# Performance work log

Measured on AMD Instinct MI355X. Metric: run time of the kernel, lower is better.

The kernel has to match this reference:

```python
import jax, jax.numpy as jnp
import numpy as np

B = 16384   # number of cells
SD = 1024   # spatial_dim
TD = 1024   # temporal_dim
FD = 1024   # fusion_dim
H = 8       # num_attention_heads


def setup_inputs() -> dict:
    key = jax.random.key(0)
    ks = jax.random.split(key, 40)
    it = iter(range(40))

    def w(o, i):
        return jax.random.normal(ks[next(it)], (o, i), dtype=jnp.float32) * 0.02

    def b(o):
        return jnp.zeros((o,), dtype=jnp.float32)

    d = {
        "spatial_features": jax.random.normal(ks[next(it)], (B, SD), dtype=jnp.float32),
        "temporal_features": jax.random.normal(ks[next(it)], (B, TD), dtype=jnp.float32),
        "sp_w": w(FD, SD), "sp_b": b(FD),
        "tp_w": w(FD, TD), "tp_b": b(FD),
    }
    for pre in ("st", "ts", "sa"):  # spatial->temporal, temporal->spatial, self
        for nm in ("q", "k", "v", "o"):
            d[f"{pre}_{nm}w"] = w(FD, FD)
            d[f"{pre}_{nm}b"] = b(FD)
    d["f1_w"] = w(FD, 2 * FD); d["f1_b"] = b(FD)
    d["f2_w"] = w(FD, FD);     d["f2_b"] = b(FD)
    d["ln_g"] = jnp.ones((FD,), jnp.float32)
    d["ln_b"] = jnp.zeros((FD,), jnp.float32)
    return d


def _mha(xq, xk, xv, qw, qb, kw, kb, vw, vb, ow, ob):
    # xq: [B, Lq, D]; xk/xv: [B, Lk, D]
    Bx, Lq, D = xq.shape
    Lk = xk.shape[1]
    hd = D // H
    Q = (xq @ qw.T + qb).reshape(Bx, Lq, H, hd)
    K = (xk @ kw.T + kb).reshape(Bx, Lk, H, hd)
    V = (xv @ vw.T + vb).reshape(Bx, Lk, H, hd)
    scores = jnp.einsum("bqhd,bkhd->bhqk", Q, K) / jnp.sqrt(jnp.float32(hd))
    attn = jax.nn.softmax(scores, axis=-1)
    out = jnp.einsum("bhqk,bkhd->bqhd", attn, V).reshape(Bx, Lq, D)
    return out @ ow.T + ob


def reference(spatial_features, temporal_features,
              sp_w, sp_b, tp_w, tp_b,
              st_qw, st_qb, st_kw, st_kb, st_vw, st_vb, st_ow, st_ob,
              ts_qw, ts_qb, ts_kw, ts_kb, ts_vw, ts_vb, ts_ow, ts_ob,
              sa_qw, sa_qb, sa_kw, sa_kb, sa_vw, sa_vb, sa_ow, sa_ob,
              f1_w, f1_b, f2_w, f2_b, ln_g, ln_b):
    # projections to fusion dim, add seq_len=1 axis
    sp = (spatial_features @ sp_w.T + sp_b)[:, None, :]   # [B,1,F]
    tp = (temporal_features @ tp_w.T + tp_b)[:, None, :]  # [B,1,F]

    # cross attention
    s_att = _mha(sp, tp, tp, st_qw, st_qb, st_kw, st_kb, st_vw, st_vb, st_ow, st_ob)[:, 0, :]
    t_att = _mha(tp, sp, sp, ts_qw, ts_qb, ts_kw, ts_kb, ts_vw, ts_vb, ts_ow, ts_ob)[:, 0, :]

    # concat fusion MLP
    cat = jnp.concatenate([s_att, t_att], axis=-1)        # [B,2F]
    fused = jax.nn.relu(cat @ f1_w.T + f1_b) @ f2_w.T + f2_b

    # self attention over seq_len=1
    fe = fused[:, None, :]
    fused = _mha(fe, fe, fe, sa_qw, sa_qb, sa_kw, sa_kb, sa_vw, sa_vb, sa_ow, sa_ob)[:, 0, :]

    # layer norm (eps matches torch default 1e-5)
    mu = jnp.mean(fused, axis=-1, keepdims=True)
    var = jnp.mean(jnp.square(fused - mu), axis=-1, keepdims=True)
    return (fused - mu) * jax.lax.rsqrt(var + 1e-5) * ln_g + ln_b
```

## Files before the change

### kernel.cpp

```cpp
#include <hip/hip_runtime.h>
#include <hip/hip_fp16.h>


typedef _Float16 half8 __attribute__((ext_vector_type(8)));
typedef float floatx4 __attribute__((ext_vector_type(4)));

#define GLOBAL_AS __attribute__((address_space(1)))
#define LDS_AS __attribute__((address_space(3)))

#define NB 16384
#define FDIM 1024

#define SBAR() asm volatile("s_barrier" ::: "memory")
#define WAIT_LGKM0() asm volatile("s_waitcnt lgkmcnt(0)" ::: "memory")
#define WAIT_VM(n) asm volatile("s_waitcnt vmcnt(" #n ")" ::: "memory")
#define SB0() __builtin_amdgcn_sched_barrier(0)
#define DSREAD(dst, addr) asm volatile("ds_read_b128 %0, %1" : "=v"(dst) : "v"(addr))

template <int RELU>
__global__ __launch_bounds__(512, 2) void gemm256(
    const _Float16* __restrict__ A, const _Float16* __restrict__ W,
    const float* __restrict__ bias, _Float16* __restrict__ C,
    int M, int N, int K, int ldc) {
  __shared__ __align__(16) _Float16 smem[2 * 2 * 256 * 64];

  const int t = threadIdx.x;
  const int lane = t & 63;
  const int w = t >> 6;
  const int wr = w >> 2;
  const int wc = w & 3;

  const int nwg = gridDim.x;
  const int bid = blockIdx.x;
  const int swz = (bid & 7) * (nwg >> 3) + (bid >> 3);
  const int nTN = N >> 8;
  const int m0 = (swz / nTN) << 8;
  const int n0 = (swz % nTN) << 8;
  const int NT = K >> 6;

  const int srow = w * 16 + (lane >> 3);
  const int scs = (lane & 7) ^ ((lane >> 3) & 7);
  const char* gA = (const char*)(A + (long)(m0 + srow) * K + scs * 8);
  const char* gB = (const char*)(W + (long)(n0 + srow) * K + scs * 8);
  const long dJ = (long)K * 16;
  const long dH = (long)K * 256;
  const int ldst = w * 2048 + lane * 16;

  unsigned sb = (unsigned)(unsigned long long)(LDS_AS void*)smem;
  const int frow = lane & 15;
  const unsigned offk = (unsigned)((((lane >> 4) * 16) ^ ((frow & 7) << 4)));
  const unsigned aoff = (unsigned)((wr * 128 + frow) * 128);
  const unsigned boff = (unsigned)(32768 + (wc * 64 + frow) * 128);

  floatx4 acc[8][4] = {};
  half8 b[4][2], aP[2][2], aQ[2][2];

#define STAGE(ab, hf, buf, gp, kb)                                               \
  do {                                                                           \
    const char* _s = (gp) + (hf) * dH + (kb);                                    \
    char* _d = (char*)smem + (buf) * 65536 + (ab) * 32768 + (hf) * 16384 + ldst; \
    __builtin_amdgcn_global_load_lds((const GLOBAL_AS void*)_s,                  \
                                     (LDS_AS void*)_d, 16, 0, 0);                \
    __builtin_amdgcn_global_load_lds((const GLOBAL_AS void*)(_s + dJ),           \
                                     (LDS_AS void*)(_d + 1024), 16, 0, 0);       \
  } while (0)

#define RD_B()                                                                    \
  do {                                                                            \
    _Pragma("unroll") for (int c = 0; c < 4; ++c) {                               \
      DSREAD(b[c][0], baseB + c * 2048 + offk);                                   \
      DSREAD(b[c][1], baseB + c * 2048 + (offk ^ 64u));                           \
    }                                                                             \
  } while (0)

#define RD_A(S, r, ba)                                                            \
  do {                                                                            \
    DSREAD(S[0][0], (ba) + (r) * 2048 + offk);                                    \
    DSREAD(S[0][1], (ba) + (r) * 2048 + (offk ^ 64u));                            \
    DSREAD(S[1][0], (ba) + (r + 1) * 2048 + offk);                                \
    DSREAD(S[1][1], (ba) + (r + 1) * 2048 + (offk ^ 64u));                        \
  } while (0)

#define QUAD(S, i0, i1)                                                                     \
  do {                                                                                      \
    __builtin_amdgcn_s_setprio(1);                                                          \
    _Pragma("unroll") for (int c = 0; c < 4; ++c) {                                         \
      acc[i0][c] = __builtin_amdgcn_mfma_f32_16x16x32_f16(S[0][0], b[c][0], acc[i0][c], 0, 0, 0); \
      acc[i0][c] = __builtin_amdgcn_mfma_f32_16x16x32_f16(S[0][1], b[c][1], acc[i0][c], 0, 0, 0); \
      acc[i1][c] = __builtin_amdgcn_mfma_f32_16x16x32_f16(S[1][0], b[c][0], acc[i1][c], 0, 0, 0); \
      acc[i1][c] = __builtin_amdgcn_mfma_f32_16x16x32_f16(S[1][1], b[c][1], acc[i1][c], 0, 0, 0); \
    }                                                                                       \
    __builtin_amdgcn_s_setprio(0);                                                          \
  } while (0)

  {
    const long k1 = 128L;
    STAGE(0, 0, 0, gA, 0); STAGE(0, 1, 0, gA, 0);
    STAGE(1, 0, 0, gB, 0); STAGE(1, 1, 0, gB, 0);
    STAGE(1, 0, 1, gB, k1); STAGE(1, 1, 1, gB, k1);
  }
  WAIT_VM(4);
  SBAR();
  RD_A(aP, 0, sb + aoff);

  for (int kt = 0; kt < NT; ++kt) {
    const int cur = kt & 1, nxt = cur ^ 1;
    const unsigned baseA = sb + (unsigned)(cur * 65536) + aoff;
    const unsigned baseAn = sb + (unsigned)(nxt * 65536) + aoff;
    const unsigned baseB = sb + (unsigned)(cur * 65536) + boff;
    const long kb1 = (long)(kt + 1 < NT ? kt + 1 : NT - 1) * 128;
    const long kb2 = (long)(kt + 2 < NT ? kt + 2 : NT - 1) * 128;

    RD_B();
    STAGE(0, 0, nxt, gA, kb1);
    SBAR(); WAIT_LGKM0();
    RD_A(aQ, 2, baseA);
    SB0();
    QUAD(aP, 0, 1);
    SBAR();

    STAGE(0, 1, nxt, gA, kb1);
    SBAR(); WAIT_LGKM0();
    RD_A(aP, 4, baseA);
    SB0();
    QUAD(aQ, 2, 3);
    SBAR();

    STAGE(1, 0, cur, gB, kb2);
    SBAR(); WAIT_LGKM0();
    RD_A(aQ, 6, baseA);
    SB0();
    QUAD(aP, 4, 5);
    SBAR();

    STAGE(1, 1, cur, gB, kb2);
    WAIT_VM(4);
    SBAR(); WAIT_LGKM0();
    RD_A(aP, 0, baseAn);
    SB0();
    QUAD(aQ, 6, 7);
    SBAR();
  }
  WAIT_VM(0);
  WAIT_LGKM0();

  const int rbase = (lane >> 4) * 4;
#pragma unroll
  for (int c = 0; c < 4; ++c) {
    const int col = n0 + wc * 64 + c * 16 + frow;
    const float bv = bias[col];
#pragma unroll
    for (int r = 0; r < 8; ++r) {
#pragma unroll
      for (int j = 0; j < 4; ++j) {
        int row = m0 + wr * 128 + r * 16 + rbase + j;
        float v = acc[r][c][j] + bv;
        if (RELU) v = fmaxf(v, 0.f);
        C[(long)row * ldc + col] = (_Float16)v;
      }
    }
  }
#undef STAGE
#undef RD_B
#undef RD_A
#undef QUAD
}

struct CVE { const float* in; _Float16* out; long ld_in; long ld_out; long n4; };
struct CVB { CVE e[7]; };
__global__ __launch_bounds__(256) void cvt_batch(CVB a) {
  const CVE e = a.e[blockIdx.y];
  long i = (long)blockIdx.x * blockDim.x + threadIdx.x;
  long stride = (long)gridDim.x * blockDim.x;
  for (; i < e.n4; i += stride) {
    long row = i >> 8;
    long c4 = i & 255;
    float4 v = *reinterpret_cast<const float4*>(e.in + row * e.ld_in + c4 * 4);
    union { _Float16 h[4]; short4 s; } u;
    u.h[0] = (_Float16)v.x; u.h[1] = (_Float16)v.y;
    u.h[2] = (_Float16)v.z; u.h[3] = (_Float16)v.w;
    *reinterpret_cast<short4*>(e.out + row * e.ld_out + c4 * 4) = u.s;
  }
}

struct TP8 { const float* in[8]; _Float16* out[8]; };
__global__ __launch_bounds__(256) void transpose_cvt(TP8 args) {
  __shared__ float tile[32][33];
  const float* in = args.in[blockIdx.z];
  _Float16* out = args.out[blockIdx.z];
  const int bx = blockIdx.x * 32;
  const int by = blockIdx.y * 32;
  const int tx = threadIdx.x & 31;
  const int ty = threadIdx.x >> 5;
#pragma unroll
  for (int r = 0; r < 32; r += 8)
    tile[ty + r][tx] = in[(long)(by + ty + r) * 1024 + bx + tx];
  __syncthreads();
#pragma unroll
  for (int r = 0; r < 32; r += 8)
    out[(long)(bx + ty + r) * 1024 + by + tx] = (_Float16)tile[tx][ty + r];
}

struct MVE { const float* W; const float* x; const float* add; float* y; long ld; int kj; };
struct MVB { MVE e[3]; };
__global__ __launch_bounds__(256) void matvecb(MVB a) {
  const MVE e = a.e[blockIdx.y];
  const int row = blockIdx.x * 4 + (threadIdx.x >> 6);
  const int lane = threadIdx.x & 63;
  const float* wr = e.W + (long)row * e.ld;
  float s = 0.f;
  for (int j = 0; j < e.kj; ++j) {
    float4 w4 = *reinterpret_cast<const float4*>(wr + (lane + 64 * j) * 4);
    float4 x4 = *reinterpret_cast<const float4*>(e.x + (lane + 64 * j) * 4);
    s += w4.x * x4.x + w4.y * x4.y + w4.z * x4.z + w4.w * x4.w;
  }
#pragma unroll
  for (int off = 32; off > 0; off >>= 1) s += __shfl_down(s, off);
  if (lane == 0) e.y[row] = s + (e.add ? e.add[row] : 0.f);
}

struct GemmArgs { const _Float16* A; const _Float16* W; const float* bias; _Float16* C; int ldc; };
struct GB5 { GemmArgs g[5]; };

__global__ __launch_bounds__(256, 2) void gemm_f16(GB5 args, int M, int N, int K) {
  __shared__ __align__(16) _Float16 As[128 * 32];
  __shared__ __align__(16) _Float16 Ws[128 * 32];

  const GemmArgs ga = args.g[blockIdx.y];
  const int t = threadIdx.x;
  const int lane = t & 63;
  const int wave = t >> 6;
  const int wr = wave >> 1;
  const int wc = wave & 1;

  const int nwg = gridDim.x;
  const int bid = blockIdx.x;
  const int swz = (bid & 7) * (nwg >> 3) + (bid >> 3);
  const int nTilesN = N >> 7;
  const int m0 = (swz / nTilesN) << 7;
  const int n0 = (swz % nTilesN) << 7;

  floatx4 acc[4][4] = {};
  const int srow = t >> 2;
  const int scol = (t & 3) * 8;
  const _Float16* Ag = ga.A + (long)(m0 + srow) * K + scol;
  const _Float16* Wg = ga.W + (long)(n0 + srow) * K + scol;
  const int frow = lane & 15;
  const int fk = (lane >> 4) * 8;

  for (int k0 = 0; k0 < K; k0 += 32) {
#pragma unroll
    for (int i = 0; i < 2; ++i) {
      __builtin_amdgcn_global_load_lds(
          (const GLOBAL_AS void*)(Ag + (long)i * 64 * K + k0),
          (LDS_AS void*)(&As[i * 2048 + t * 8]), 16, 0, 0);
      __builtin_amdgcn_global_load_lds(
          (const GLOBAL_AS void*)(Wg + (long)i * 64 * K + k0),
          (LDS_AS void*)(&Ws[i * 2048 + t * 8]), 16, 0, 0);
    }
    __syncthreads();
    half8 a[4], b[4];
#pragma unroll
    for (int r = 0; r < 4; ++r)
      a[r] = *(const half8*)&As[(wr * 64 + r * 16 + frow) * 32 + fk];
#pragma unroll
    for (int c = 0; c < 4; ++c)
      b[c] = *(const half8*)&Ws[(wc * 64 + c * 16 + frow) * 32 + fk];
#pragma unroll
    for (int r = 0; r < 4; ++r)
#pragma unroll
      for (int c = 0; c < 4; ++c)
        acc[r][c] = __builtin_amdgcn_mfma_f32_16x16x32_f16(a[r], b[c], acc[r][c], 0, 0, 0);
    __syncthreads();
  }

  const int rbase = lane >> 4;
#pragma unroll
  for (int c = 0; c < 4; ++c) {
    const int col = n0 + wc * 64 + c * 16 + frow;
    const float bv = ga.bias ? ga.bias[col] : 0.f;
#pragma unroll
    for (int r = 0; r < 4; ++r)
#pragma unroll
      for (int j = 0; j < 4; ++j) {
        int row = m0 + wr * 64 + r * 16 + rbase * 4 + j;
        ga.C[(long)row * ga.ldc + col] = (_Float16)(acc[r][c][j] + bv);
      }
  }
}

__global__ __launch_bounds__(256) void ln_f16(const _Float16* __restrict__ x,
                                              const float* __restrict__ g,
                                              const float* __restrict__ b,
                                              float* __restrict__ out) {
  const int row = blockIdx.x;
  const int t = threadIdx.x;
  const _Float16* xr = x + (size_t)row * FDIM;
  short4 raw = reinterpret_cast<const short4*>(xr)[t];
  union { short4 s; _Float16 h[4]; } u;
  u.s = raw;
  float v0 = (float)u.h[0], v1 = (float)u.h[1], v2 = (float)u.h[2], v3 = (float)u.h[3];
  float s = v0 + v1 + v2 + v3;
  float q = v0 * v0 + v1 * v1 + v2 * v2 + v3 * v3;
#pragma unroll
  for (int off = 32; off > 0; off >>= 1) {
    s += __shfl_down(s, off);
    q += __shfl_down(q, off);
  }
  __shared__ float ss[4], qs[4];
  int wave = t >> 6, lane = t & 63;
  if (lane == 0) { ss[wave] = s; qs[wave] = q; }
  __syncthreads();
  float S = ss[0] + ss[1] + ss[2] + ss[3];
  float Q = qs[0] + qs[1] + qs[2] + qs[3];
  float mu = S * (1.f / FDIM);
  float var = Q * (1.f / FDIM) - mu * mu;
  float rs = rsqrtf(var + 1e-5f);
  int c = t * 4;
  float4 o;
  o.x = (v0 - mu) * rs * g[c + 0] + b[c + 0];
  o.y = (v1 - mu) * rs * g[c + 1] + b[c + 1];
  o.z = (v2 - mu) * rs * g[c + 2] + b[c + 2];
  o.w = (v3 - mu) * rs * g[c + 3] + b[c + 3];
  reinterpret_cast<float4*>(out + (size_t)row * FDIM)[t] = o;
}

extern "C" void kernel_launch(void* const* d_in, const int* in_sizes, int n_in,
                              void* d_out, int out_size, void* d_ws, size_t ws_size,
                              hipStream_t stream) {
  const float* spatial  = (const float*)d_in[0];
  const float* temporal = (const float*)d_in[1];
  const float* sp_w = (const float*)d_in[2];
  const float* sp_b = (const float*)d_in[3];
  const float* tp_w = (const float*)d_in[4];
  const float* tp_b = (const float*)d_in[5];
  const float* st_vw = (const float*)d_in[10];
  const float* st_vb = (const float*)d_in[11];
  const float* st_ow = (const float*)d_in[12];
  const float* st_ob = (const float*)d_in[13];
  const float* ts_vw = (const float*)d_in[18];
  const float* ts_vb = (const float*)d_in[19];
  const float* ts_ow = (const float*)d_in[20];
  const float* ts_ob = (const float*)d_in[21];
  const float* sa_vw = (const float*)d_in[26];
  const float* sa_vb = (const float*)d_in[27];
  const float* sa_ow = (const float*)d_in[28];
  const float* sa_ob = (const float*)d_in[29];
  const float* f1_w = (const float*)d_in[30];
  const float* f1_b = (const float*)d_in[31];
  const float* f2_w = (const float*)d_in[32];
  const float* f2_b = (const float*)d_in[33];
  const float* ln_g = (const float*)d_in[34];
  const float* ln_b = (const float*)d_in[35];

  char* base = (char*)d_ws;
  size_t off = 0;
  auto alloc = [&](size_t bytes) { void* p = base + off; off += (bytes + 255) & ~255ull; return p; };
  const size_t W16 = 1024 * 1024 * sizeof(_Float16);

  _Float16* Xcat = (_Float16*)alloc((size_t)NB * 2048 * 2);
  _Float16* h    = (_Float16*)alloc((size_t)NB * 1024 * 2);
  _Float16* opre = (_Float16*)alloc((size_t)NB * 1024 * 2);
  _Float16* st_owT = (_Float16*)alloc(W16);
  _Float16* ts_owT = (_Float16*)alloc(W16);
  _Float16* sa_vwT = (_Float16*)alloc(W16);
  _Float16* tp_wT  = (_Float16*)alloc(W16);
  _Float16* sp_wT  = (_Float16*)alloc(W16);
  _Float16* f2_wT  = (_Float16*)alloc(W16);
  _Float16* f1a16  = (_Float16*)alloc(W16);
  _Float16* f1b16  = (_Float16*)alloc(W16);
  _Float16* sa_ow16= (_Float16*)alloc(W16);
  _Float16* st_vw16= (_Float16*)alloc(W16);
  _Float16* ts_vw16= (_Float16*)alloc(W16);
  _Float16* P1 = (_Float16*)alloc(W16);
  _Float16* Q2 = (_Float16*)alloc(W16);
  _Float16* P3 = (_Float16*)alloc(W16);
  _Float16* Q4 = (_Float16*)alloc(W16);
  _Float16* P5 = (_Float16*)alloc(W16);
  _Float16* W2 = (_Float16*)alloc(W16);
  _Float16* Wh = (_Float16*)alloc((size_t)1024 * 2048 * 2);
  float* u1 = (float*)alloc(3 * 1024 * 4);
  float* u2 = (float*)alloc(3 * 1024 * 4);
  float* bh = (float*)alloc(1024 * 4);

  {
    CVB cb = {};
    cb.e[0] = { temporal, Xcat,        1024, 2048, (long)NB * 256 };
    cb.e[1] = { spatial,  Xcat + 1024, 1024, 2048, (long)NB * 256 };
    cb.e[2] = { f1_w,        f1a16,   2048, 1024, 1024 * 256 };
    cb.e[3] = { f1_w + 1024, f1b16,   2048, 1024, 1024 * 256 };
    cb.e[4] = { sa_ow,       sa_ow16, 1024, 1024, 1024 * 256 };
    cb.e[5] = { st_vw,       st_vw16, 1024, 1024, 1024 * 256 };
    cb.e[6] = { ts_vw,       ts_vw16, 1024, 1024, 1024 * 256 };
    cvt_batch<<<dim3(1024, 7), 256, 0, stream>>>(cb);
  }

  TP8 tp = {};
  tp.in[0] = st_ow; tp.out[0] = st_owT;
  tp.in[1] = ts_ow; tp.out[1] = ts_owT;
  tp.in[2] = sa_vw; tp.out[2] = sa_vwT;
  tp.in[3] = tp_w;  tp.out[3] = tp_wT;
  tp.in[4] = sp_w;  tp.out[4] = sp_wT;
  tp.in[5] = f2_w;  tp.out[5] = f2_wT;
  transpose_cvt<<<dim3(32, 32, 6), 256, 0, stream>>>(tp);

  {
    MVB a = {};
    a.e[0] = { st_vw, tp_b, st_vb, u1,        1024, 4 };
    a.e[1] = { ts_vw, sp_b, ts_vb, u1 + 1024, 1024, 4 };
    a.e[2] = { sa_vw, f2_b, sa_vb, u1 + 2048, 1024, 4 };
    matvecb<<<dim3(256, 3), 256, 0, stream>>>(a);
  }
  {
    MVB a = {};
    a.e[0] = { st_ow, u1,        st_ob, u2,        1024, 4 };
    a.e[1] = { ts_ow, u1 + 1024, ts_ob, u2 + 1024, 1024, 4 };
    a.e[2] = { sa_ow, u1 + 2048, sa_ob, u2 + 2048, 1024, 4 };
    matvecb<<<dim3(256, 3), 256, 0, stream>>>(a);
  }
  {
    MVB a = {};
    a.e[0] = { f1_w, u2, f1_b, bh, 2048, 8 };
    matvecb<<<dim3(256, 1), 256, 0, stream>>>(a);
  }

  {
    GB5 g = {};
    g.g[0] = { f1a16,  st_owT, nullptr, P1, 1024 };
    g.g[1] = { tp_wT,  st_vw16, nullptr, Q2, 1024 };
    g.g[2] = { f1b16,  ts_owT, nullptr, P3, 1024 };
    g.g[3] = { sp_wT,  ts_vw16, nullptr, Q4, 1024 };
    g.g[4] = { sa_ow16, sa_vwT, nullptr, P5, 1024 };
    gemm_f16<<<dim3(64, 5), 256, 0, stream>>>(g, 1024, 1024, 1024);
  }
  {
    GB5 g = {};
    g.g[0] = { P1, Q2, nullptr, Wh,        2048 };
    g.g[1] = { P3, Q4, nullptr, Wh + 1024, 2048 };
    g.g[2] = { P5, f2_wT, nullptr, W2,     1024 };
    gemm_f16<<<dim3(64, 3), 256, 0, stream>>>(g, 1024, 1024, 1024);
  }

  gemm256<1><<<dim3(256), 512, 0, stream>>>(Xcat, Wh, bh, h, NB, 1024, 2048, 1024);
  gemm256<0><<<dim3(256), 512, 0, stream>>>(h, W2, u2 + 2048, opre, NB, 1024, 1024, 1024);

  ln_f16<<<NB, 256, 0, stream>>>(opre, ln_g, ln_b, (float*)d_out);
}
```

Before: 233.9 us.

## Prefetch A two k-tiles ahead and load all A fragments early in GEMM loop

Reworks the GEMM main loop so A tiles are staged two k-steps ahead, like B, instead of one, and each iteration reads all eight A fragment pairs from LDS in two batches rather than ping-ponging two register sets. The MFMA order inside each quad is regrouped so that consecutive MFMAs use independent accumulators. The goal is to cut exposed global-load latency and LDS-read waits between MFMA blocks. In exchange it uses more VGPRs for A fragments, which under launch_bounds(512,2) could cause spills, and it overwrites LDS buffers in place, which needs correct barrier ordering.

```diff
diff --git a/kernel.cpp b/kernel.cpp
--- a/kernel.cpp
+++ b/kernel.cpp
@@ -53,7 +53,7 @@
   const unsigned boff = (unsigned)(32768 + (wc * 64 + frow) * 128);
 
   floatx4 acc[8][4] = {};
-  half8 b[4][2], aP[2][2], aQ[2][2];
+  half8 b[4][2], a0[2][2], a1[2][2], a2[2][2], a3[2][2];
 
 #define STAGE(ab, hf, buf, gp, kb)                                               \
   do {                                                                           \
@@ -84,12 +84,14 @@
 #define QUAD(S, i0, i1)                                                                     \
   do {                                                                                      \
     __builtin_amdgcn_s_setprio(1);                                                          \
-    _Pragma("unroll") for (int c = 0; c < 4; ++c) {                                         \
+    _Pragma("unroll") for (int c = 0; c < 4; ++c)                                           \
       acc[i0][c] = __builtin_amdgcn_mfma_f32_16x16x32_f16(S[0][0], b[c][0], acc[i0][c], 0, 0, 0); \
+    _Pragma("unroll") for (int c = 0; c < 4; ++c)                                           \
+      acc[i1][c] = __builtin_amdgcn_mfma_f32_16x16x32_f16(S[1][0], b[c][0], acc[i1][c], 0, 0, 0); \
+    _Pragma("unroll") for (int c = 0; c < 4; ++c)                                           \
       acc[i0][c] = __builtin_amdgcn_mfma_f32_16x16x32_f16(S[0][1], b[c][1], acc[i0][c], 0, 0, 0); \
-      acc[i1][c] = __builtin_amdgcn_mfma_f32_16x16x32_f16(S[1][0], b[c][0], acc[i1][c], 0, 0, 0); \
+    _Pragma("unroll") for (int c = 0; c < 4; ++c)                                           \
       acc[i1][c] = __builtin_amdgcn_mfma_f32_16x16x32_f16(S[1][1], b[c][1], acc[i1][c], 0, 0, 0); \
-    }                                                                                       \
     __builtin_amdgcn_s_setprio(0);                                                          \
   } while (0)
 
@@ -97,48 +99,43 @@
     const long k1 = 128L;
     STAGE(0, 0, 0, gA, 0); STAGE(0, 1, 0, gA, 0);
     STAGE(1, 0, 0, gB, 0); STAGE(1, 1, 0, gB, 0);
+    STAGE(0, 0, 1, gA, k1); STAGE(0, 1, 1, gA, k1);
     STAGE(1, 0, 1, gB, k1); STAGE(1, 1, 1, gB, k1);
   }
-  WAIT_VM(4);
+  WAIT_VM(8);
   SBAR();
-  RD_A(aP, 0, sb + aoff);
 
   for (int kt = 0; kt < NT; ++kt) {
-    const int cur = kt & 1, nxt = cur ^ 1;
+    const int cur = kt & 1;
     const unsigned baseA = sb + (unsigned)(cur * 65536) + aoff;
-    const unsigned baseAn = sb + (unsigned)(nxt * 65536) + aoff;
     const unsigned baseB = sb + (unsigned)(cur * 65536) + boff;
-    const long kb1 = (long)(kt + 1 < NT ? kt + 1 : NT - 1) * 128;
     const long kb2 = (long)(kt + 2 < NT ? kt + 2 : NT - 1) * 128;
 
     RD_B();
-    STAGE(0, 0, nxt, gA, kb1);
-    SBAR(); WAIT_LGKM0();
-    RD_A(aQ, 2, baseA);
+    RD_A(a0, 0, baseA);
+    RD_A(a1, 2, baseA);
+    SBAR(); WAIT_LGKM0(); SB0();
+    QUAD(a0, 0, 1);
+    SBAR();
+
+    STAGE(1, 0, cur, gB, kb2);
+    SBAR();
+    RD_A(a2, 4, baseA);
+    RD_A(a3, 6, baseA);
     SB0();
-    QUAD(aP, 0, 1);
+    QUAD(a1, 2, 3);
     SBAR();
 
-    STAGE(0, 1, nxt, gA, kb1);
-    SBAR(); WAIT_LGKM0();
-    RD_A(aP, 4, baseA);
-    SB0();
-    QUAD(aQ, 2, 3);
+    STAGE(1, 1, cur, gB, kb2);
+    SBAR(); WAIT_LGKM0(); SB0();
+    QUAD(a2, 4, 5);
     SBAR();
 
-    STAGE(1, 0, cur, gB, kb2);
-    SBAR(); WAIT_LGKM0();
-    RD_A(aQ, 6, baseA);
-    SB0();
-    QUAD(aP, 4, 5);
-    SBAR();
-
-    STAGE(1, 1, cur, gB, kb2);
-    WAIT_VM(4);
-    SBAR(); WAIT_LGKM0();
-    RD_A(aP, 0, baseAn);
-    SB0();
-    QUAD(aQ, 6, 7);
+    STAGE(0, 0, cur, gA, kb2);
+    STAGE(0, 1, cur, gA, kb2);
+    WAIT_VM(8);
+    SBAR(); SB0();
+    QUAD(a3, 6, 7);
     SBAR();
   }
   WAIT_VM(0);
```

Result: no change. 238.1 us (+1.8%).
